# Kernel optimization log

Hardware: AMD Instinct MI355X
Metric: run time of the kernel (lower is better)

The kernel has to match this reference:

```python
import jax, jax.numpy as jnp
import numpy as np

HIDDEN = 8   # TrajGRU hidden channels (hardcoded in module)
L = 5        # number of flow links
NEG = 0.2    # leaky relu slope (HKO-7 RNN_ACT_TYPE)


def conv2d(x, w, b, pad):
    y = jax.lax.conv_general_dilated(x, w, (1, 1), [(pad, pad), (pad, pad)],
                                     dimension_numbers=('NCHW', 'OIHW', 'NCHW'))
    return y + b[None, :, None, None]


def leaky(x):
    return jnp.where(x >= 0, x, NEG * x)


def bilinear_sample(im, x, y):
    # im: (C,H,W); x,y: (H,W) pixel coords; zero padding outside (grid_sample align_corners=True)
    C, H, W = im.shape
    x0 = jnp.floor(x); y0 = jnp.floor(y)
    wx = x - x0; wy = y - y0

    def g(ix, iy):
        valid = (ix >= 0) & (ix <= W - 1) & (iy >= 0) & (iy <= H - 1)
        ic = jnp.clip(ix, 0, W - 1).astype(jnp.int32)
        jc = jnp.clip(iy, 0, H - 1).astype(jnp.int32)
        return jnp.where(valid[None], im[:, jc, ic], 0.0)

    v00 = g(x0, y0); v01 = g(x0 + 1, y0)
    v10 = g(x0, y0 + 1); v11 = g(x0 + 1, y0 + 1)
    top = v00 * (1 - wx) + v01 * wx
    bot = v10 * (1 - wx) + v11 * wx
    return top * (1 - wy) + bot * wy


def trajgru_step(x, h, w_i2h, b_i2h, w_i2f, b_i2f, w_h2f, b_h2f,
                 w_flows, b_flows, w_ret, b_ret):
    B, C, H, W = h.shape
    # flow generator
    f = leaky(conv2d(x, w_i2f, b_i2f, 2) + conv2d(h, w_h2f, b_h2f, 2))
    flows = conv2d(f, w_flows, b_flows, 2).reshape(B, L, 2, H, W)
    # warp hidden along each link: wrap(h, -flow) => sample at grid - flow
    xx = jnp.arange(W, dtype=jnp.float32)[None, :] * jnp.ones((H, 1), jnp.float32)
    yy = jnp.arange(H, dtype=jnp.float32)[:, None] * jnp.ones((1, W), jnp.float32)
    cx = xx - flows[:, :, 0]  # (B,L,H,W)
    cy = yy - flows[:, :, 1]
    warp_b = jax.vmap(lambda hb, cxb, cyb:
                      jax.vmap(lambda a, b2: bilinear_sample(hb, a, b2))(cxb, cyb))
    warped = warp_b(h, cx, cy).reshape(B, L * C, H, W)  # (B, L*C, H, W)
    h2h = conv2d(warped, w_ret, b_ret, 0)
    i2h = conv2d(x, w_i2h, b_i2h, 1)
    i_r, i_u, i_m = jnp.split(i2h, 3, axis=1)
    h_r, h_u, h_m = jnp.split(h2h, 3, axis=1)
    reset = jax.nn.sigmoid(i_r + h_r)
    update = jax.nn.sigmoid(i_u + h_u)
    new_mem = leaky(i_m + reset * h_m)
    return update * h + (1.0 - update) * new_mem


def setup_inputs():
    key = jax.random.key(0)
    ks = jax.random.split(key, 16)
    B, T_in, T_out, H, W = 32, 12, 12, 128, 128
    in_ch = T_in + T_out
    p = lambda k, shape: 0.1 * jax.random.normal(k, shape, dtype=jnp.float32)
    return {
        'radar_data': jax.random.normal(ks[0], (B, T_in, 1, H, W), dtype=jnp.float32),
        'first_stage_pred': jax.random.normal(ks[1], (B, T_out, 1, H, W), dtype=jnp.float32),
        'w_conv_in': p(ks[2], (HIDDEN, in_ch, 3, 3)), 'b_conv_in': p(ks[3], (HIDDEN,)),
        'w_i2h': p(ks[4], (3 * HIDDEN, HIDDEN, 3, 3)), 'b_i2h': p(ks[5], (3 * HIDDEN,)),
        'w_i2f': p(ks[6], (32, HIDDEN, 5, 5)), 'b_i2f': p(ks[7], (32,)),
        'w_h2f': p(ks[8], (32, HIDDEN, 5, 5)), 'b_h2f': p(ks[9], (32,)),
        'w_flows': p(ks[10], (2 * L, 32, 5, 5)), 'b_flows': p(ks[11], (2 * L,)),
        'w_ret': p(ks[12], (3 * HIDDEN, L * HIDDEN, 1, 1)), 'b_ret': p(ks[13], (3 * HIDDEN,)),
        'w_conv_out': p(ks[14], (T_out, HIDDEN, 1, 1)), 'b_conv_out': p(ks[15], (T_out,)),
    }


def reference(radar_data, first_stage_pred, w_conv_in, b_conv_in, w_i2h, b_i2h,
              w_i2f, b_i2f, w_h2f, b_h2f, w_flows, b_flows, w_ret, b_ret,
              w_conv_out, b_conv_out):
    B, T_in, _, H, W = radar_data.shape
    T_out = first_stage_pred.shape[1]
    x = jnp.concatenate([radar_data.reshape(B, T_in, H, W),
                         first_stage_pred.reshape(B, T_out, H, W)], axis=1)
    x = conv2d(x, w_conv_in, b_conv_in, 1)          # (B, hidden, H, W)
    h0 = jnp.zeros((B, HIDDEN, H, W), x.dtype)       # TrajGRU zero initial state
    h = trajgru_step(x, h0, w_i2h, b_i2h, w_i2f, b_i2f, w_h2f, b_h2f,
                     w_flows, b_flows, w_ret, b_ret)  # seq_len == 1
    out = conv2d(h, w_conv_out, b_conv_out, 0)       # (B, pred_len, H, W)
    return out.reshape(B, T_out, 1, H, W)
```

## Files before the change

### kernel.cpp

```cpp
#include <hip/hip_runtime.h>
#include <hip/hip_bf16.h>


typedef __fp16   h2f __attribute__((ext_vector_type(2)));
typedef _Float16 v8h __attribute__((ext_vector_type(8)));
typedef float    v4f __attribute__((ext_vector_type(4)));

#define HW 128
#define SPITCH 40

#define WB_HOFF 4608
#define FLT_OFF 16384
#define N_PREP  7820

__global__ __launch_bounds__(256)
void prep(const float* __restrict__ w_in,  const float* __restrict__ b_in,
          const float* __restrict__ w_i2h, const float* __restrict__ b_i2h,
          const float* __restrict__ b_ret, const float* __restrict__ w_out,
          const float* __restrict__ b_out, void* __restrict__ ws)
{
    int idx = blockIdx.x * 256 + threadIdx.x;
    _Float16* wh = (_Float16*)ws;
    float* fw = (float*)((char*)ws + FLT_OFF);
    if (idx < 4608) {
        int j = idx & 7, r = idx >> 3;
        int lane = r & 63, s = r >> 6;
        int quad = lane >> 4, n = lane & 15;
        int ch = quad * 8 + j;
        float v = 0.f;
        if (n < 8) {
            if (ch < 24)                 v = w_in[n*216 + ch*9 + s];
            else if (ch == 24 && s == 4) v = b_in[n];
        }
        wh[idx] = (_Float16)v;
    } else if (idx < 7680) {
        int i2 = idx - 4608;
        int j = i2 & 7, r = i2 >> 3;
        int lane = r & 63; r >>= 6;
        int nt = r & 1, s = r >> 1;
        int quad = lane >> 4, n = lane & 15;
        int kk = s * 32 + quad * 8 + j;
        int t = kk >> 3, m = kk & 7;
        int o = nt * 16 + n;
        float v = (t < 9 && o < 24) ? w_i2h[o*72 + m*9 + t] : 0.f;
        wh[WB_HOFF + i2] = (_Float16)v;
    } else if (idx < N_PREP) {
        int j = idx - 7680;
        float v;
        if (j < 32) {
            int c = j & 7, sel = j >> 3;
            v = (sel==0) ? b_i2h[c]    + b_ret[c]
              : (sel==1) ? b_i2h[8+c]  + b_ret[8+c]
              : (sel==2) ? b_i2h[16+c] : b_ret[16+c];
        } else if (j < 128) v = w_out[j-32];
        else                v = b_out[j-128];
        fw[j] = v;
    }
}

__device__ __forceinline__ void pack_store(_Float16* dst, const float* v, bool ones)
{
    union { h2f h2[16]; v8h h8[4]; } u;
#pragma unroll
    for (int k = 0; k < 12; ++k)
        u.h2[k] = __builtin_amdgcn_cvt_pkrtz(v[2 * k], v[2 * k + 1]);
    u.h2[12] = __builtin_amdgcn_cvt_pkrtz(ones ? 1.f : 0.f, 0.f);
#pragma unroll
    for (int k = 13; k < 16; ++k) u.h2[k] = (h2f)0.f;
#pragma unroll
    for (int k = 0; k < 4; ++k) *(v8h*)&dst[8 * k] = u.h8[k];
}

__global__ __launch_bounds__(256, 5)
void radar2_mfma(const float* __restrict__ radar,
                 const float* __restrict__ pred,
                 const void*  __restrict__ ws,
                 float* __restrict__ out)
{
    __shared__ __align__(16) char pool[400 * SPITCH * 2];
    _Float16* s_in = (_Float16*)pool;
    _Float16* s_x  = (_Float16*)pool;
    float*    s_hc = (float*)(pool + 5376);

    const _Float16* wh = (const _Float16*)ws;
    const float* fw = (const float*)((const char*)ws + FLT_OFF);

    const int tid  = threadIdx.x;
    const int lane = tid & 63;
    const int wave = tid >> 6;
    const int quad = lane >> 4;
    const int col  = lane & 15;

    const int id   = blockIdx.x;
    const int b    = (id & 7) * 4 + ((id >> 3) >> 6);
    const int tile = (id >> 3) & 63;
    const int ty0  = (tile >> 3) << 4;
    const int tx0  = (tile & 7) << 4;

    const float* rb = radar + (((size_t)b * 12) << 14);
    const float* pb = pred  + (((size_t)b * 12) << 14);

    const int r0 = tid, r1 = tid + 256;
    const int ly0 = r0 / 20, lx0 = r0 - 20 * ly0;
    const int gy0 = ty0 + ly0 - 2, gx0 = tx0 + lx0 - 2;
    const bool in0 = ((unsigned)gy0 < HW) & ((unsigned)gx0 < HW);
    const int off0 = (gy0 << 7) + gx0;
    const bool has1 = (r1 < 400);
    const int ly1 = r1 / 20, lx1 = r1 - 20 * ly1;
    const int gy1 = ty0 + ly1 - 2, gx1 = tx0 + lx1 - 2;
    const bool in1 = has1 & ((unsigned)gy1 < HW) & ((unsigned)gx1 < HW);
    const int off1 = (gy1 << 7) + gx1;

    float va[24], vb24[24];
#pragma unroll
    for (int c = 0; c < 12; ++c) {
        va[c]      = in0 ? rb[((size_t)c << 14) + off0] : 0.f;
        va[12 + c] = in0 ? pb[((size_t)c << 14) + off0] : 0.f;
    }
#pragma unroll
    for (int c = 0; c < 12; ++c) {
        vb24[c]      = in1 ? rb[((size_t)c << 14) + off1] : 0.f;
        vb24[12 + c] = in1 ? pb[((size_t)c << 14) + off1] : 0.f;
    }
    pack_store(&s_in[r0 * SPITCH], va, in0);
    if (has1) pack_store(&s_in[r1 * SPITCH], vb24, in1);

    v8h bfA[9];
#pragma unroll
    for (int s = 0; s < 9; ++s) bfA[s] = *(const v8h*)&wh[(s * 64 + lane) * 8];
    __syncthreads();

    int pbase[6];
#pragma unroll
    for (int t = 0; t < 6; ++t) {
        int p = (wave + 4 * t) * 16 + col; if (p > 323) p = 323;
        pbase[t] = ((p / 18) * 20 + (p % 18)) * SPITCH + quad * 8;
    }
    v4f accA[6];
#pragma unroll
    for (int t = 0; t < 6; ++t) accA[t] = (v4f){0.f, 0.f, 0.f, 0.f};
#pragma unroll
    for (int t = 0; t < 6; ++t) {
        if (wave + 4 * t < 21) {
#pragma unroll
            for (int s = 0; s < 9; ++s) {
                v8h a = *(const v8h*)&s_in[pbase[t] + ((s / 3) * 20 + (s % 3)) * SPITCH];
                accA[t] = __builtin_amdgcn_mfma_f32_16x16x32_f16(a, bfA[s], accA[t], 0, 0, 0);
            }
        }
    }
    __syncthreads();

    if (col < 8) {
#pragma unroll
        for (int t = 0; t < 6; ++t) {
            int mt = wave + 4 * t;
            if (mt < 21) {
#pragma unroll
                for (int r = 0; r < 4; ++r) {
                    int pa = mt * 16 + quad * 4 + r;
                    int py = pa / 18, px = pa - 18 * py;
                    bool ok = (pa < 324) &&
                              ((unsigned)(ty0 + py - 1) < HW) &&
                              ((unsigned)(tx0 + px - 1) < HW);
                    s_x[pa * 8 + col] = (_Float16)(ok ? accA[t][r] : 0.f);
                }
            }
        }
    }
    __syncthreads();

    int toff2[3];
#pragma unroll
    for (int s = 0; s < 3; ++s) {
        int t = s * 4 + quad;
        toff2[s] = (t < 9) ? ((t / 3) * 18 + (t % 3)) * 8 : 0;
    }
    v8h bfB[3][2];
#pragma unroll
    for (int s = 0; s < 3; ++s)
#pragma unroll
        for (int nt = 0; nt < 2; ++nt)
            bfB[s][nt] = *(const v8h*)&wh[WB_HOFF + ((s * 2 + nt) * 64 + lane) * 8];

    v4f acc0[4], acc1[4];
#pragma unroll
    for (int t = 0; t < 4; ++t) {
        acc0[t] = (v4f){0.f, 0.f, 0.f, 0.f};
        acc1[t] = (v4f){0.f, 0.f, 0.f, 0.f};
    }
#pragma unroll
    for (int t = 0; t < 4; ++t) {
        int abase = ((wave + 4 * t) * 18 + col) * 8;
#pragma unroll
        for (int s = 0; s < 3; ++s) {
            v8h a = *(const v8h*)&s_x[abase + toff2[s]];
            acc0[t] = __builtin_amdgcn_mfma_f32_16x16x32_f16(a, bfB[s][0], acc0[t], 0, 0, 0);
            acc1[t] = __builtin_amdgcn_mfma_f32_16x16x32_f16(a, bfB[s][1], acc1[t], 0, 0, 0);
        }
    }

    const int c7 = lane & 7;
    const float g0v = fw[c7], g1v = fw[8 + c7], g2v = fw[16 + c7], g3v = fw[24 + c7];
#pragma unroll
    for (int t = 0; t < 4; ++t) {
        int mt = wave + 4 * t;
#pragma unroll
        for (int r = 0; r < 4; ++r) {
            float iu = __shfl_xor(acc0[t][r], 8, 64);
            if (col < 8) {
                float rr = 1.f / (1.f + __expf(-(acc0[t][r] + g0v)));
                float uu = 1.f / (1.f + __expf(-(iu + g1v)));
                float mm = acc1[t][r] + g2v + rr * g3v;
                mm = (mm >= 0.f) ? mm : 0.2f * mm;
                s_hc[(mt * 16 + quad * 4 + r) * 9 + c7] = (1.f - uu) * mm;
            }
        }
    }
    __syncthreads();

    float h[8];
#pragma unroll
    for (int c = 0; c < 8; ++c) h[c] = s_hc[tid * 9 + c];
    const float* wout = fw + 32;
    const float* bout = fw + 128;
    const int oy = tid >> 4, ox = tid & 15;
    float* op = out + (((size_t)b * 12) << 14) + ((ty0 + oy) << 7) + (tx0 + ox);
#pragma unroll
    for (int t = 0; t < 12; ++t) {
        float o = bout[t];
#pragma unroll
        for (int c = 0; c < 8; ++c) o = fmaf(h[c], wout[t * 8 + c], o);
        op[(size_t)t << 14] = o;
    }
}

extern "C" void kernel_launch(void* const* d_in, const int* in_sizes, int n_in,
                              void* d_out, int out_size, void* d_ws, size_t ws_size,
                              hipStream_t stream) {
    (void)in_sizes; (void)n_in; (void)ws_size; (void)out_size;
    const float* radar = (const float*)d_in[0];
    const float* pred  = (const float*)d_in[1];
    const float* w_in  = (const float*)d_in[2];
    const float* b_in  = (const float*)d_in[3];
    const float* w_i2h = (const float*)d_in[4];
    const float* b_i2h = (const float*)d_in[5];
    const float* b_ret = (const float*)d_in[13];
    const float* w_out = (const float*)d_in[14];
    const float* b_out = (const float*)d_in[15];

    prep<<<(N_PREP + 255) / 256, 256, 0, stream>>>(w_in, b_in, w_i2h, b_i2h,
                                                   b_ret, w_out, b_out, d_ws);

    radar2_mfma<<<dim3(2048), dim3(256), 0, stream>>>(radar, pred, d_ws, (float*)d_out);
}
```

Measured before the change: 139.9 us.

## Shrink input-conv LDS pitch and regroup MFMA K by tap-channel groups

Reduces the staged input pixel pitch from 40 to 24 halves by dropping the ones/bias channel and padding. The conv_in bias is now added in the epilogue instead. The MFMA K dimension is reorganised so each quad handles a different tap and the 24 channels are split into three 8-channel groups, with weights re-packed to match. The MFMA count stays at 9 per tile, and the smaller LDS footprint allows raising the occupancy hint to 8 blocks per CU, at the cost of more register pressure.

Result: slower. 167.3 us (+19.6%).

```diff
diff --git a/kernel.cpp b/kernel.cpp
--- a/kernel.cpp
+++ b/kernel.cpp
@@ -7,11 +7,11 @@
 typedef float    v4f __attribute__((ext_vector_type(4)));
 
 #define HW 128
-#define SPITCH 40
+#define SPITCH 24
 
 #define WB_HOFF 4608
 #define FLT_OFF 16384
-#define N_PREP  7820
+#define N_PREP  7828
 
 __global__ __launch_bounds__(256)
 void prep(const float* __restrict__ w_in,  const float* __restrict__ b_in,
@@ -24,14 +24,11 @@
     float* fw = (float*)((char*)ws + FLT_OFF);
     if (idx < 4608) {
         int j = idx & 7, r = idx >> 3;
-        int lane = r & 63, s = r >> 6;
+        int lane = r & 63, sg = r >> 6;
+        int g = sg % 3, s = sg / 3;
         int quad = lane >> 4, n = lane & 15;
-        int ch = quad * 8 + j;
-        float v = 0.f;
-        if (n < 8) {
-            if (ch < 24)                 v = w_in[n*216 + ch*9 + s];
-            else if (ch == 24 && s == 4) v = b_in[n];
-        }
+        int tap = s * 4 + quad;
+        float v = (n < 8 && tap < 9) ? w_in[n*216 + (g*8 + j)*9 + tap] : 0.f;
         wh[idx] = (_Float16)v;
     } else if (idx < 7680) {
         int i2 = idx - 4608;
@@ -53,25 +50,23 @@
               : (sel==1) ? b_i2h[8+c]  + b_ret[8+c]
               : (sel==2) ? b_i2h[16+c] : b_ret[16+c];
         } else if (j < 128) v = w_out[j-32];
-        else                v = b_out[j-128];
+        else if (j < 140)   v = b_out[j-128];
+        else                v = b_in[j-140];
         fw[j] = v;
     }
 }
 
-__device__ __forceinline__ void pack_store(_Float16* dst, const float* v, bool ones)
+__device__ __forceinline__ void pack_store(_Float16* dst, const float* v)
 {
-    union { h2f h2[16]; v8h h8[4]; } u;
+    union { h2f h2[12]; v8h h8[3]; } u;
 #pragma unroll
     for (int k = 0; k < 12; ++k)
         u.h2[k] = __builtin_amdgcn_cvt_pkrtz(v[2 * k], v[2 * k + 1]);
-    u.h2[12] = __builtin_amdgcn_cvt_pkrtz(ones ? 1.f : 0.f, 0.f);
-#pragma unroll
-    for (int k = 13; k < 16; ++k) u.h2[k] = (h2f)0.f;
-#pragma unroll
-    for (int k = 0; k < 4; ++k) *(v8h*)&dst[8 * k] = u.h8[k];
-}
-
-__global__ __launch_bounds__(256, 5)
+#pragma unroll
+    for (int k = 0; k < 3; ++k) *(v8h*)&dst[8 * k] = u.h8[k];
+}
+
+__global__ __launch_bounds__(256, 8)
 void radar2_mfma(const float* __restrict__ radar,
                  const float* __restrict__ pred,
                  const void*  __restrict__ ws,
@@ -122,19 +117,25 @@
         vb24[c]      = in1 ? rb[((size_t)c << 14) + off1] : 0.f;
         vb24[12 + c] = in1 ? pb[((size_t)c << 14) + off1] : 0.f;
     }
-    pack_store(&s_in[r0 * SPITCH], va, in0);
-    if (has1) pack_store(&s_in[r1 * SPITCH], vb24, in1);
+    pack_store(&s_in[r0 * SPITCH], va);
+    if (has1) pack_store(&s_in[r1 * SPITCH], vb24);
 
     v8h bfA[9];
 #pragma unroll
-    for (int s = 0; s < 9; ++s) bfA[s] = *(const v8h*)&wh[(s * 64 + lane) * 8];
-    __syncthreads();
-
+    for (int i = 0; i < 9; ++i) bfA[i] = *(const v8h*)&wh[(i * 64 + lane) * 8];
+    __syncthreads();
+
+    int toffA[3];
+#pragma unroll
+    for (int s = 0; s < 3; ++s) {
+        int t = s * 4 + quad;
+        toffA[s] = (t < 9) ? ((t / 3) * 20 + (t % 3)) * SPITCH : 0;
+    }
     int pbase[6];
 #pragma unroll
     for (int t = 0; t < 6; ++t) {
         int p = (wave + 4 * t) * 16 + col; if (p > 323) p = 323;
-        pbase[t] = ((p / 18) * 20 + (p % 18)) * SPITCH + quad * 8;
+        pbase[t] = ((p / 18) * 20 + (p % 18)) * SPITCH;
     }
     v4f accA[6];
 #pragma unroll
@@ -143,14 +144,19 @@
     for (int t = 0; t < 6; ++t) {
         if (wave + 4 * t < 21) {
 #pragma unroll
-            for (int s = 0; s < 9; ++s) {
-                v8h a = *(const v8h*)&s_in[pbase[t] + ((s / 3) * 20 + (s % 3)) * SPITCH];
-                accA[t] = __builtin_amdgcn_mfma_f32_16x16x32_f16(a, bfA[s], accA[t], 0, 0, 0);
+            for (int s = 0; s < 3; ++s) {
+                int ab = pbase[t] + toffA[s];
+#pragma unroll
+                for (int g = 0; g < 3; ++g) {
+                    v8h a = *(const v8h*)&s_in[ab + g * 8];
+                    accA[t] = __builtin_amdgcn_mfma_f32_16x16x32_f16(a, bfA[s * 3 + g], accA[t], 0, 0, 0);
+                }
             }
         }
     }
     __syncthreads();
 
+    const float binv = fw[140 + (col & 7)];
     if (col < 8) {
 #pragma unroll
         for (int t = 0; t < 6; ++t) {
@@ -163,7 +169,7 @@
                     bool ok = (pa < 324) &&
                               ((unsigned)(ty0 + py - 1) < HW) &&
                               ((unsigned)(tx0 + px - 1) < HW);
-                    s_x[pa * 8 + col] = (_Float16)(ok ? accA[t][r] : 0.f);
+                    s_x[pa * 8 + col] = (_Float16)(ok ? accA[t][r] + binv : 0.f);
                 }
             }
         }
```
